# Performance work log

Hardware: AMD Instinct MI355X
Metric: run time of the kernel (lower is better)

The kernel has to match this reference:

```python
import jax, jax.numpy as jnp
import numpy as np

T, L, H, C, D_IN, ED, N, E = 4, 3, 1, 256, 20, 10, 4096, 65536
D = H * C  # 256, pooling width
AH = 4     # pooling attention heads


def setup_inputs() -> dict:
    key = jax.random.key(0)
    ks = jax.random.split(key, 24)
    g = lambda k, s, sc=0.05: jax.random.normal(k, s, jnp.float32) * sc
    return {
        "x": jax.random.normal(ks[0], (N, D_IN), jnp.float32),
        "src": jax.random.randint(ks[1], (E,), 0, N),
        "dst": jax.random.randint(ks[2], (E,), 0, N),
        "edge_attr": jax.random.normal(ks[3], (E, ED), jnp.float32),
        "edge_type": jax.random.randint(ks[4], (E,), 0, T),
        # GATConv params per (edge_type, layer)
        "W0": g(ks[5], (T, D_IN, H * C)),          # layer 0 lin
        "W12": g(ks[6], (T, 2, H * C, H * C)),     # layers 1,2 lin
        "att_src": g(ks[7], (T, L, H, C)),
        "att_dst": g(ks[8], (T, L, H, C)),
        "att_edge": g(ks[9], (T, L, H, C)),
        "lin_edge_w": g(ks[10], (T, L, ED, H * C)),
        "biases": g(ks[11], (T, L, C)),            # H=1 so concat/mean both give C
        "edge_type_weights": jnp.ones((T,), jnp.float32) / T,
        # pooling: MultiheadAttention(D, 4 heads)
        "in_proj_w": g(ks[12], (3 * D, D)),
        "in_proj_b": g(ks[13], (3 * D,)),
        "out_proj_w": g(ks[14], (D, D)),
        "out_proj_b": g(ks[15], (D,)),
        # fusion MLP: 3D -> 2D -> 256
        "fus_w1": g(ks[16], (3 * D, 2 * D)),
        "fus_b1": g(ks[17], (2 * D,)),
        "fus_w2": g(ks[18], (2 * D, 256)),
        "fus_b2": g(ks[19], (256,)),
    }


def _gat(h, src, dst, mask, e_attr, W, a_s, a_d, a_e, We, b, concat):
    # PyG GATConv (edge_dim, add_self_loops=True, fill_value='mean'), eval mode
    Nn = h.shape[0]
    Hh, Cc = a_s.shape
    xl = (h @ W).reshape(Nn, Hh, Cc)
    s_src = jnp.sum(xl * a_s, -1)   # [N,H]
    s_dst = jnp.sum(xl * a_d, -1)   # [N,H]
    s_e = jnp.sum((e_attr @ We).reshape(-1, Hh, Cc) * a_e, -1)  # [E,H]
    # self-loop edge_attr = per-node mean of masked incoming edge_attr
    m = mask.astype(h.dtype)
    cnt = jax.ops.segment_sum(m, dst, Nn)
    loop_attr = jax.ops.segment_sum(e_attr * m[:, None], dst, Nn) / jnp.maximum(cnt, 1.0)[:, None]
    s_loop = jnp.sum((loop_attr @ We).reshape(Nn, Hh, Cc) * a_e, -1)  # [N,H]
    a_real = jax.nn.leaky_relu(s_src[src] + s_dst[dst] + s_e, 0.2)
    a_real = jnp.where(mask[:, None], a_real, -1e30)  # mask edges not of this type
    a_loop = jax.nn.leaky_relu(s_src + s_dst + s_loop, 0.2)
    ar = jnp.arange(Nn)
    idx = jnp.concatenate([dst, ar])    # destination of each (edge + self-loop)
    sidx = jnp.concatenate([src, ar])   # source of each
    scores = jnp.concatenate([a_real, a_loop], 0)  # [E+N, H]
    smax = jax.ops.segment_max(scores, idx, Nn)
    ex = jnp.exp(scores - smax[idx])
    ssum = jax.ops.segment_sum(ex, idx, Nn)
    alpha = ex / (ssum[idx] + 1e-16)
    out = jax.ops.segment_sum(xl[sidx] * alpha[:, :, None], idx, Nn)  # [N,H,C]
    out = out.reshape(Nn, Hh * Cc) if concat else out.mean(1)
    return out + b


def reference(x, src, dst, edge_attr, edge_type, W0, W12, att_src, att_dst,
              att_edge, lin_edge_w, biases, edge_type_weights, in_proj_w,
              in_proj_b, out_proj_w, out_proj_b, fus_w1, fus_b1, fus_w2, fus_b2):
    outs = []
    for t in range(T):
        mask = edge_type == t
        h = x
        for i in range(L):
            W = W0[t] if i == 0 else W12[t, i - 1]
            h = _gat(h, src, dst, mask, edge_attr, W, att_src[t, i],
                     att_dst[t, i], att_edge[t, i], lin_edge_w[t, i],
                     biases[t, i], concat=(i < L - 1))
            h = jax.nn.elu(h)  # dropout off in eval
        outs.append(h)
    w = jax.nn.softmax(edge_type_weights)
    h = sum(w[t] * outs[t] for t in range(T))  # [N, D]
    # HierarchicalGraphPooling
    mean_p = h.mean(0)
    max_p = h.max(0)
    qkv = h @ in_proj_w.T + in_proj_b
    q, k, v = jnp.split(qkv, 3, axis=-1)
    HD = D // AH
    q = q.reshape(-1, AH, HD)
    k = k.reshape(-1, AH, HD)
    v = v.reshape(-1, AH, HD)
    att = jax.nn.softmax(jnp.einsum('nhd,mhd->hnm', q, k) / np.float32(np.sqrt(HD)), axis=-1)
    o = jnp.einsum('hnm,mhd->nhd', att, v).reshape(-1, D) @ out_proj_w.T + out_proj_b
    attn_p = o.mean(0)
    comb = jnp.concatenate([mean_p, max_p, attn_p])  # [3D]
    g = jax.nn.relu(comb @ fus_w1 + fus_b1)
    g = jax.nn.relu(g @ fus_w2 + fus_b2)
    return g[None, :]
```

## Files before the change

### kernel.cpp

```cpp
#include <hip/hip_runtime.h>
#include <math.h>

#define T 4
#define LL 3
#define C 256
#define DIN 20
#define NN 4096
#define EE 65536
#define AHD 4
#define MCH 8
#define QKS 72
#define AST 264
#define SLOTN (16384*64)

#define W_CURSOR 0
#define W_SLSRC  16384
#define F_SLSE   (W_SLSRC + SLOTN)
#define F_XL     (F_SLSE + 3*SLOTN)
#define F_H      (F_XL + T*NN*C)
#define F_OPART  F_XL
#define F_SSRC   (F_H + T*NN*C)
#define F_SDST   (F_SSRC + T*NN)
#define F_WE     (F_SDST + T*NN)
#define F_HACC   (F_WE + 128)
#define F_WT     (F_HACC + NN*C)
#define F_QKV    (F_WT + 768*256)
#define F_DPART  (F_QKV + NN*768)
#define F_MEANP  (F_DPART + MCH*NN*AHD)
#define F_MAXP   (F_MEANP + C)
#define F_OMEAN  (F_MAXP + C)
#define F_ATTNP  (F_OMEAN + C)
#define F_G1     (F_ATTNP + C)
#define U_W12P   (F_G1 + 512)
#define WS_WORDS (U_W12P + 262144)

static __device__ __forceinline__ float lrelu(float x){ return x > 0.f ? x : 0.2f*x; }
static __device__ __forceinline__ float eluf(float x){ return x > 0.f ? x : __expf(x) - 1.f; }

typedef _Float16 half2_t __attribute__((ext_vector_type(2)));
typedef _Float16 v8h __attribute__((ext_vector_type(8)));
typedef float v4f __attribute__((ext_vector_type(4)));

static __device__ __forceinline__ unsigned pk2(float x, float y){
  half2_t h; h.x = (_Float16)x; h.y = (_Float16)y;
  return __builtin_bit_cast(unsigned, h);
}

static __device__ inline void atomicMaxF(float* addr, float val){
  int* ai = (int*)addr;
  int old = __float_as_int(*addr);
  while (__int_as_float(old) < val){
    int assumed = old;
    old = atomicCAS(ai, assumed, __float_as_int(val));
    if (old == assumed) break;
  }
}

__global__ __launch_bounds__(256) void prep_k(
    const float* __restrict__ x, const float* __restrict__ W0,
    const float* __restrict__ attS, const float* __restrict__ attD,
    float* __restrict__ xlo, float* __restrict__ ssrc, float* __restrict__ sdst,
    const float* __restrict__ w12, _Float16* __restrict__ wpT,
    const float* __restrict__ ipw, _Float16* __restrict__ ip16,
    const float* __restrict__ linE, const float* __restrict__ attE,
    float* we, float* fbase, int* cursor){
  __shared__ float smem[64*65];
  __shared__ float red[64];
  int by = blockIdx.y, bx = blockIdx.x, tid = threadIdx.x;
  if (by < 4){
    int t = by;
    const float* W = W0 + (size_t)t*DIN*C;
    int n0 = bx*8;
    for (int j = 0; j < 8; j++)
      for (int k = tid; k < DIN; k += 256)
        smem[j*DIN + k] = x[(n0+j)*DIN + k];
    __syncthreads();
    float acc[8] = {0,0,0,0,0,0,0,0};
    int c = tid;
    for (int k = 0; k < DIN; k += 4){
      float w0 = W[(k+0)*C + c], w1 = W[(k+1)*C + c], w2 = W[(k+2)*C + c], w3 = W[(k+3)*C + c];
      #pragma unroll
      for (int j = 0; j < 8; j++){
        float4 h4 = *(const float4*)&smem[j*DIN + k];
        acc[j] += w0*h4.x + w1*h4.y + w2*h4.z + w3*h4.w;
      }
    }
    #pragma unroll
    for (int j = 0; j < 8; j++) xlo[((size_t)t*NN + n0 + j)*C + c] = acc[j];
    float aS = attS[t*LL*C + c], aD = attD[t*LL*C + c];
    int lane = c & 63, w = c >> 6;
    #pragma unroll
    for (int j = 0; j < 8; j++){
      float v1 = acc[j]*aS, v2 = acc[j]*aD;
      #pragma unroll
      for (int off = 32; off > 0; off >>= 1){ v1 += __shfl_down(v1, off); v2 += __shfl_down(v2, off); }
      if (lane == 0){ red[j*8 + w] = v1; red[j*8 + 4 + w] = v2; }
    }
    __syncthreads();
    if (c < 16){
      int j = c >> 1, which = c & 1;
      const float* r = red + j*8 + which*4;
      float s = r[0] + r[1] + r[2] + r[3];
      (which ? sdst : ssrc)[t*NN + n0 + j] = s;
    }
  } else if (by < 12){
    if (bx < 16){
      int b8 = by - 4;
      int k0 = (bx >> 2)*64, n0 = (bx & 3)*64;
      const float* src = w12 + ((size_t)b8*256 + k0)*256 + n0;
      int row = tid >> 2, l4 = (tid & 3)*4;
      #pragma unroll
      for (int pass = 0; pass < 4; pass++){
        float4 v = *(const float4*)(src + (size_t)row*256 + pass*16 + l4);
        int o = row*65 + pass*16 + l4;
        smem[o+0] = v.x; smem[o+1] = v.y; smem[o+2] = v.z; smem[o+3] = v.w;
      }
      __syncthreads();
      int n = tid >> 2, seg = tid & 3;
      _Float16* dstp = wpT + ((size_t)b8*256 + n0 + n)*256 + k0 + seg*16;
      v8h h0, h1;
      #pragma unroll
      for (int i = 0; i < 8; i++) h0[i] = (_Float16)smem[(seg*16 + i)*65 + n];
      #pragma unroll
      for (int i = 0; i < 8; i++) h1[i] = (_Float16)smem[(seg*16 + 8 + i)*65 + n];
      *(v8h*)(dstp) = h0;
      *(v8h*)(dstp + 8) = h1;
    }
  } else if (by < 15){
    if (bx < 256){
      int j = (by - 12)*256 + bx;
      ip16[(size_t)j*256 + tid] = (_Float16)ipw[(size_t)j*256 + tid];
    }
  } else {
    if (bx < 12){
      int t = bx / 3, l = bx % 3;
      float ae = attE[(t*LL + l)*C + tid];
      const float* lw = linE + (size_t)((t*LL + l)*10)*C;
      for (int k = 0; k < 10; k++) smem[k*C + tid] = lw[k*C + tid]*ae;
      __syncthreads();
      if (tid < 10){
        float s = 0.f;
        for (int i = 0; i < C; i++) s += smem[tid*C + i];
        we[(t*LL + l)*10 + tid] = s;
      }
    } else if (bx == 12){
      fbase[tid] = 0.f;
      fbase[256 + tid] = -1e30f;
      fbase[512 + tid] = 0.f;
    } else if (bx >= 64 && bx < 128){
      cursor[(bx - 64)*256 + tid] = 0;
    }
  }
}

__global__ __launch_bounds__(256) void scat_k(const int* __restrict__ dst, const int* __restrict__ ety,
                                              const int* __restrict__ srcv, const float* __restrict__ eattr,
                                              const float* __restrict__ we,
                                              int* cursor, int* slot_src, float* slot_se){
  int e = blockIdx.x*256 + threadIdx.x;
  if (e < EE){
    int t = ety[e];
    int gid = dst[e]*T + t;
    int p = atomicAdd(&cursor[gid], 1);
    if (p < 64){
      int sl = gid*64 + p;
      slot_src[sl] = srcv[e];
      float ea[10];
      #pragma unroll
      for (int k = 0; k < 10; k++) ea[k] = eattr[(size_t)e*10 + k];
      #pragma unroll
      for (int l = 0; l < 3; l++){
        const float* w = we + (t*LL + l)*10;
        float s = 0.f;
        #pragma unroll
        for (int k = 0; k < 10; k++) s += ea[k]*w[k];
        slot_se[(size_t)l*SLOTN + sl] = s;
      }
    }
  }
}

__global__ __launch_bounds__(256, 2) void gemm16m_k(const float* __restrict__ hin,
                                                    const _Float16* __restrict__ wpT,
                                                    const float* __restrict__ attS, const float* __restrict__ attD,
                                                    int l, float* __restrict__ xlo,
                                                    float* __restrict__ ssrc, float* __restrict__ sdst){
  __shared__ __align__(16) _Float16 As[64*AST];
  __shared__ float redS[4*64], redD[4*64];
  int t = blockIdx.y;
  int mb = blockIdx.x*64;
  int tid = threadIdx.x;
  int w = tid >> 6, lane = tid & 63;
  int r16 = lane & 15, q = lane >> 4;
  const float* h = hin + ((size_t)t*NN + mb)*C;
  {
    int sr = tid >> 2, sc = (tid & 3)*64;
    const float* hr = h + (size_t)sr*C + sc;
    #pragma unroll
    for (int i = 0; i < 8; i++){
      float4 a = *(const float4*)(hr + 8*i);
      float4 b = *(const float4*)(hr + 8*i + 4);
      v8h hv = {(_Float16)a.x,(_Float16)a.y,(_Float16)a.z,(_Float16)a.w,
                (_Float16)b.x,(_Float16)b.y,(_Float16)b.z,(_Float16)b.w};
      *(v8h*)(As + (size_t)sr*AST + sc + 8*i) = hv;
    }
  }
  __syncthreads();
  int cb = w*64;
  const _Float16* WB = wpT + ((size_t)((t*2 + (l-1))*256 + cb))*256;
  v4f o[4][4];
  #pragma unroll
  for (int i = 0; i < 4; i++)
    #pragma unroll
    for (int j = 0; j < 4; j++) o[i][j] = (v4f){0.f,0.f,0.f,0.f};
  #pragma unroll
  for (int kk = 0; kk < 8; kk++){
    v8h a[4], b[4];
    #pragma unroll
    for (int mi = 0; mi < 4; mi++) a[mi] = *(v8h*)(As + (size_t)(mi*16 + r16)*AST + kk*32 + q*8);
    #pragma unroll
    for (int ni = 0; ni < 4; ni++) b[ni] = *(const v8h*)(WB + (size_t)(ni*16 + r16)*256 + kk*32 + q*8);
    #pragma unroll
    for (int mi = 0; mi < 4; mi++)
      #pragma unroll
      for (int ni = 0; ni < 4; ni++)
        o[mi][ni] = __builtin_amdgcn_mfma_f32_16x16x32_f16(a[mi], b[ni], o[mi][ni], 0, 0, 0);
  }
  int tl = t*LL + l;
  float aS[4], aD[4];
  #pragma unroll
  for (int ni = 0; ni < 4; ni++){
    aS[ni] = attS[tl*C + cb + ni*16 + r16];
    aD[ni] = attD[tl*C + cb + ni*16 + r16];
  }
  #pragma unroll
  for (int mi = 0; mi < 4; mi++)
    #pragma unroll
    for (int rr = 0; rr < 4; rr++){
      int row = mb + mi*16 + q*4 + rr;
      float v1 = 0.f, v2 = 0.f;
      #pragma unroll
      for (int ni = 0; ni < 4; ni++){
        float ov = o[mi][ni][rr];
        xlo[((size_t)t*NN + row)*C + cb + ni*16 + r16] = ov;
        v1 += ov*aS[ni]; v2 += ov*aD[ni];
      }
      v1 += __shfl_xor(v1, 1); v2 += __shfl_xor(v2, 1);
      v1 += __shfl_xor(v1, 2); v2 += __shfl_xor(v2, 2);
      v1 += __shfl_xor(v1, 4); v2 += __shfl_xor(v2, 4);
      v1 += __shfl_xor(v1, 8); v2 += __shfl_xor(v2, 8);
      if (r16 == 0){
        redS[w*64 + mi*16 + q*4 + rr] = v1;
        redD[w*64 + mi*16 + q*4 + rr] = v2;
      }
    }
  __syncthreads();
  if (tid < 64)
    ssrc[t*NN + mb + tid] = redS[tid] + redS[64+tid] + redS[128+tid] + redS[192+tid];
  else if (tid < 128){
    int i = tid - 64;
    sdst[t*NN + mb + i] = redD[i] + redD[64+i] + redD[128+i] + redD[192+i];
  }
}

__global__ __launch_bounds__(256, 2) void qkv16m_k(const float* __restrict__ hacc,
                                                   const _Float16* __restrict__ ip16,
                                                   const float* __restrict__ ipb, float* __restrict__ qkv,
                                                   float* meanp, float* maxp){
  __shared__ __align__(16) _Float16 As[64*AST];
  int p = blockIdx.y;
  int mb = blockIdx.x*64;
  int tid = threadIdx.x;
  int w = tid >> 6, lane = tid & 63;
  int r16 = lane & 15, q = lane >> 4;
  {
    int sr = tid >> 2, sc = (tid & 3)*64;
    const float* hr = hacc + ((size_t)(mb + sr))*C + sc;
    #pragma unroll
    for (int i = 0; i < 8; i++){
      float4 a = *(const float4*)(hr + 8*i);
      float4 b = *(const float4*)(hr + 8*i + 4);
      v8h hv = {(_Float16)a.x,(_Float16)a.y,(_Float16)a.z,(_Float16)a.w,
                (_Float16)b.x,(_Float16)b.y,(_Float16)b.z,(_Float16)b.w};
      *(v8h*)(As + (size_t)sr*AST + sc + 8*i) = hv;
    }
  }
  __syncthreads();
  int cb = p*256 + w*64;
  v4f o[4][4];
  #pragma unroll
  for (int i = 0; i < 4; i++)
    #pragma unroll
    for (int j = 0; j < 4; j++) o[i][j] = (v4f){0.f,0.f,0.f,0.f};
  #pragma unroll
  for (int kk = 0; kk < 8; kk++){
    v8h a[4], b[4];
    #pragma unroll
    for (int mi = 0; mi < 4; mi++) a[mi] = *(v8h*)(As + (size_t)(mi*16 + r16)*AST + kk*32 + q*8);
    #pragma unroll
    for (int ni = 0; ni < 4; ni++) b[ni] = *(const v8h*)(ip16 + (size_t)(cb + ni*16 + r16)*256 + kk*32 + q*8);
    #pragma unroll
    for (int mi = 0; mi < 4; mi++)
      #pragma unroll
      for (int ni = 0; ni < 4; ni++)
        o[mi][ni] = __builtin_amdgcn_mfma_f32_16x16x32_f16(a[mi], b[ni], o[mi][ni], 0, 0, 0);
  }
  float bn[4];
  #pragma unroll
  for (int ni = 0; ni < 4; ni++) bn[ni] = ipb[cb + ni*16 + r16];
  #pragma unroll
  for (int mi = 0; mi < 4; mi++)
    #pragma unroll
    for (int rr = 0; rr < 4; rr++){
      int row = mb + mi*16 + q*4 + rr;
      #pragma unroll
      for (int ni = 0; ni < 4; ni++)
        qkv[(size_t)row*768 + cb + ni*16 + r16] = o[mi][ni][rr] + bn[ni];
    }
  if (p == 0){
    float sm = 0.f, mx = -1e30f;
    for (int r = 0; r < 64; r++){
      float v = hacc[(size_t)(mb + r)*C + tid];
      sm += v; mx = fmaxf(mx, v);
    }
    atomicAdd(&meanp[tid], sm*(1.f/4096.f));
    atomicMaxF(&maxp[tid], mx);
  }
}

__global__ __launch_bounds__(256) void agg_k(const float* __restrict__ xl, const float* __restrict__ ssrc,
                                             const float* __restrict__ sdst,
                                             const int* __restrict__ cnt, const int* __restrict__ slot_src,
                                             const float* __restrict__ slot_se,
                                             const float* __restrict__ bias, float* __restrict__ hout,
                                             const float* __restrict__ etw, float* __restrict__ hacc, int l){
  __shared__ float4 sh[4][64];
  int gid = blockIdx.x*4 + (threadIdx.x >> 6);
  int lane = threadIdx.x & 63;
  int n = gid >> 2, t = gid & 3;
  int deg = cnt[gid];
  if (deg > 64) deg = 64;
  float sd = sdst[t*NN + n];
  float se_e = 0.f; int sj = 0;
  if (lane < deg){
    int sl = gid*64 + lane;
    sj = slot_src[sl];
    se_e = slot_se[(size_t)l*SLOTN + sl];
  }
  float ssum_se = se_e;
  #pragma unroll
  for (int o = 32; o > 0; o >>= 1) ssum_se += __shfl_xor(ssum_se, o);
  float sloop = ssum_se / (float)(deg > 0 ? deg : 1);
  float sc = (lane < deg) ? lrelu(ssrc[t*NN + sj] + sd + se_e) : -1e30f;
  float al = lrelu(ssrc[t*NN + n] + sd + sloop);
  float mx = fmaxf(sc, al);
  #pragma unroll
  for (int o = 32; o > 0; o >>= 1) mx = fmaxf(mx, __shfl_xor(mx, o));
  float ex = (lane < deg) ? __expf(sc - mx) : 0.f;
  float ale = __expf(al - mx);
  float ssum = ex;
  #pragma unroll
  for (int o = 32; o > 0; o >>= 1) ssum += __shfl_xor(ssum, o);
  float inv = 1.f/(ssum + ale + 1e-16f);
  const float4* xl4 = (const float4*)xl;
  float4 acc = xl4[((size_t)(t*NN + n))*64 + lane];
  acc.x *= ale; acc.y *= ale; acc.z *= ale; acc.w *= ale;
  int dmax = deg - 1;
  for (int j0 = 0; j0 < deg; j0 += 4){
    float p0 = __shfl(ex, j0);
    float p1 = (j0+1 < deg) ? __shfl(ex, j0+1) : 0.f;
    float p2 = (j0+2 < deg) ? __shfl(ex, j0+2) : 0.f;
    float p3 = (j0+3 < deg) ? __shfl(ex, j0+3) : 0.f;
    int s0 = __shfl(sj, j0);
    int s1 = __shfl(sj, (j0+1 < deg) ? j0+1 : dmax);
    int s2 = __shfl(sj, (j0+2 < deg) ? j0+2 : dmax);
    int s3 = __shfl(sj, (j0+3 < deg) ? j0+3 : dmax);
    float4 v0 = xl4[((size_t)(t*NN + s0))*64 + lane];
    float4 v1 = xl4[((size_t)(t*NN + s1))*64 + lane];
    float4 v2 = xl4[((size_t)(t*NN + s2))*64 + lane];
    float4 v3 = xl4[((size_t)(t*NN + s3))*64 + lane];
    acc.x += p0*v0.x + p1*v1.x + p2*v2.x + p3*v3.x;
    acc.y += p0*v0.y + p1*v1.y + p2*v2.y + p3*v3.y;
    acc.z += p0*v0.z + p1*v1.z + p2*v2.z + p3*v3.z;
    acc.w += p0*v0.w + p1*v1.w + p2*v2.w + p3*v3.w;
  }
  float4 b4 = *(const float4*)&bias[(t*LL + l)*C + lane*4];
  acc.x = eluf(acc.x*inv + b4.x); acc.y = eluf(acc.y*inv + b4.y);
  acc.z = eluf(acc.z*inv + b4.z); acc.w = eluf(acc.w*inv + b4.w);
  if (l < 2){
    ((float4*)hout)[((size_t)(t*NN + n))*64 + lane] = acc;
  } else {
    sh[t][lane] = acc;
    __syncthreads();
    if (t == 0){
      float e0 = etw[0], e1 = etw[1], e2 = etw[2], e3 = etw[3];
      float m = fmaxf(fmaxf(e0,e1), fmaxf(e2,e3));
      float w0 = __expf(e0-m), w1 = __expf(e1-m), w2 = __expf(e2-m), w3 = __expf(e3-m);
      float winv = 1.f/(w0+w1+w2+w3);
      float4 v0 = sh[0][lane], v1 = sh[1][lane], v2 = sh[2][lane], v3 = sh[3][lane];
      float4 s;
      s.x = (w0*v0.x + w1*v1.x + w2*v2.x + w3*v3.x)*winv;
      s.y = (w0*v0.y + w1*v1.y + w2*v2.y + w3*v3.y)*winv;
      s.z = (w0*v0.z + w1*v1.z + w2*v2.z + w3*v3.z)*winv;
      s.w = (w0*v0.w + w1*v1.w + w2*v2.w + w3*v3.w)*winv;
      ((float4*)hacc)[(size_t)n*64 + lane] = s;
    }
  }
}

__global__ __launch_bounds__(256, 2) void attn_k(const float* __restrict__ qkv,
                                                 float* __restrict__ opart,
                                                 float* __restrict__ dpart){
  __shared__ __align__(16) _Float16 Ks[64*QKS];
  __shared__ __align__(16) _Float16 VTs[64*QKS];
  __shared__ __align__(16) _Float16 Ps[4][64*QKS];
  int tid = threadIdx.x;
  int wave = tid >> 6, l = tid & 63;
  int nb = blockIdx.x*256 + wave*64;
  int h = blockIdx.y, mc = blockIdx.z;
  int r16 = l & 15, q = l >> 4;
  _Float16* Pw = Ps[wave];

  v8h qf[4][2];
  #pragma unroll
  for (int ni = 0; ni < 4; ni++){
    const float* qrow = qkv + (size_t)(nb + ni*16 + r16)*768 + h*64;
    #pragma unroll
    for (int kk = 0; kk < 2; kk++){
      float4 a = *(const float4*)(qrow + kk*32 + q*8);
      float4 b = *(const float4*)(qrow + kk*32 + q*8 + 4);
      v8h hv = {(_Float16)(a.x*0.125f), (_Float16)(a.y*0.125f),
                (_Float16)(a.z*0.125f), (_Float16)(a.w*0.125f),
                (_Float16)(b.x*0.125f), (_Float16)(b.y*0.125f),
                (_Float16)(b.z*0.125f), (_Float16)(b.w*0.125f)};
      qf[ni][kk] = hv;
    }
  }

  v4f o[4][4];
  #pragma unroll
  for (int i = 0; i < 4; i++)
    #pragma unroll
    for (int j = 0; j < 4; j++) o[i][j] = (v4f){0.f,0.f,0.f,0.f};
  float dn[4] = {0.f,0.f,0.f,0.f};

  for (int mt = 0; mt < NN/MCH/64; mt++){
    int mb = mc*(NN/MCH) + mt*64;
    __syncthreads();
    {
      int sr = tid >> 2, sc = (tid & 3)*16;
      const float* krow = qkv + (size_t)(mb + sr)*768 + 256 + h*64 + sc;
      float4 a = *(const float4*)(krow + 0);
      float4 b = *(const float4*)(krow + 4);
      float4 cc = *(const float4*)(krow + 8);
      float4 d = *(const float4*)(krow + 12);
      v8h h0 = {(_Float16)a.x, (_Float16)a.y, (_Float16)a.z, (_Float16)a.w,
                (_Float16)b.x, (_Float16)b.y, (_Float16)b.z, (_Float16)b.w};
      v8h h1 = {(_Float16)cc.x, (_Float16)cc.y, (_Float16)cc.z, (_Float16)cc.w,
                (_Float16)d.x, (_Float16)d.y, (_Float16)d.z, (_Float16)d.w};
      *(v8h*)(Ks + (size_t)sr*QKS + sc) = h0;
      *(v8h*)(Ks + (size_t)sr*QKS + sc + 8) = h1;
    }
    {
      int m0 = (tid & 31)*2;
      int db = (tid >> 5)*8;
      const float* v0 = qkv + (size_t)(mb + m0)*768 + 512 + h*64 + db;
      const float* v1 = v0 + 768;
      #pragma unroll
      for (int i = 0; i < 2; i++){
        float4 a = *(const float4*)(v0 + 4*i);
        float4 b = *(const float4*)(v1 + 4*i);
        int d = db + 4*i;
        *(unsigned*)(VTs + (size_t)(d+0)*QKS + m0) = pk2(a.x, b.x);
        *(unsigned*)(VTs + (size_t)(d+1)*QKS + m0) = pk2(a.y, b.y);
        *(unsigned*)(VTs + (size_t)(d+2)*QKS + m0) = pk2(a.z, b.z);
        *(unsigned*)(VTs + (size_t)(d+3)*QKS + m0) = pk2(a.w, b.w);
      }
    }
    __syncthreads();
    v4f c[4][4];
    #pragma unroll
    for (int i = 0; i < 4; i++)
      #pragma unroll
      for (int j = 0; j < 4; j++) c[i][j] = (v4f){0.f,0.f,0.f,0.f};
    #pragma unroll
    for (int kk = 0; kk < 2; kk++){
      v8h a[4];
      #pragma unroll
      for (int mi = 0; mi < 4; mi++) a[mi] = *(v8h*)(Ks + (size_t)(mi*16 + r16)*QKS + kk*32 + q*8);
      #pragma unroll
      for (int mi = 0; mi < 4; mi++)
        #pragma unroll
        for (int ni = 0; ni < 4; ni++)
          c[mi][ni] = __builtin_amdgcn_mfma_f32_16x16x32_f16(a[mi], qf[ni][kk], c[mi][ni], 0, 0, 0);
    }
    #pragma unroll
    for (int mi = 0; mi < 4; mi++)
      #pragma unroll
      for (int ni = 0; ni < 4; ni++){
        float e0 = __expf(c[mi][ni][0]), e1 = __expf(c[mi][ni][1]),
              e2 = __expf(c[mi][ni][2]), e3 = __expf(c[mi][ni][3]);
        dn[ni] += e0 + e1 + e2 + e3;
        *(uint2*)(Pw + (size_t)(ni*16 + r16)*QKS + mi*16 + q*4) = make_uint2(pk2(e0,e1), pk2(e2,e3));
      }
    #pragma unroll
    for (int km = 0; km < 2; km++){
      v8h pa[4], vb[4];
      #pragma unroll
      for (int ni = 0; ni < 4; ni++) pa[ni] = *(v8h*)(Pw + (size_t)(ni*16 + r16)*QKS + km*32 + q*8);
      #pragma unroll
      for (int di = 0; di < 4; di++) vb[di] = *(v8h*)(VTs + (size_t)(di*16 + r16)*QKS + km*32 + q*8);
      #pragma unroll
      for (int ni = 0; ni < 4; ni++)
        #pragma unroll
        for (int di = 0; di < 4; di++)
          o[ni][di] = __builtin_amdgcn_mfma_f32_16x16x32_f16(pa[ni], vb[di], o[ni][di], 0, 0, 0);
    }
  }

  float* ob = opart + ((size_t)mc*NN + nb)*C + h*64;
  #pragma unroll
  for (int ni = 0; ni < 4; ni++)
    #pragma unroll
    for (int di = 0; di < 4; di++)
      #pragma unroll
      for (int r = 0; r < 4; r++)
        ob[(size_t)(ni*16 + q*4 + r)*C + di*16 + r16] = o[ni][di][r];
  #pragma unroll
  for (int ni = 0; ni < 4; ni++){
    dn[ni] += __shfl_xor(dn[ni], 16);
    dn[ni] += __shfl_xor(dn[ni], 32);
  }
  if (q == 0){
    #pragma unroll
    for (int ni = 0; ni < 4; ni++)
      dpart[((size_t)mc*NN + nb + ni*16 + r16)*AHD + h] = dn[ni];
  }
}

__global__ __launch_bounds__(256) void attnred_k(const float* __restrict__ opart, const float* __restrict__ dpart,
                                                 float* omean){
  int r0 = blockIdx.x*(NN/256), c = threadIdx.x;
  int head = c >> 6;
  float s = 0.f;
  for (int r = 0; r < NN/256; r++){
    int n = r0 + r;
    float dsum = 0.f, osum = 0.f;
    #pragma unroll
    for (int mc = 0; mc < MCH; mc++){
      dsum += dpart[((size_t)mc*NN + n)*AHD + head];
      osum += opart[((size_t)mc*NN + n)*C + c];
    }
    s += osum / (dsum + 1e-16f);
  }
  atomicAdd(&omean[c], s*(1.f/4096.f));
}

__global__ __launch_bounds__(256) void taila_k(const float* __restrict__ omean, const float* __restrict__ opw,
                                               const float* __restrict__ opb, const float* __restrict__ fb1,
                                               float* attnp, float* g1){
  __shared__ float sh[256];
  int tid = threadIdx.x;
  sh[tid] = omean[tid];
  __syncthreads();
  int jj = tid >> 4, kk = tid & 15;
  int j = blockIdx.x*16 + jj;
  float acc = 0.f;
  #pragma unroll
  for (int i = 0; i < 16; i++){
    int k = kk*16 + i;
    acc += sh[k]*opw[(size_t)j*256 + k];
  }
  acc += __shfl_xor(acc, 1); acc += __shfl_xor(acc, 2);
  acc += __shfl_xor(acc, 4); acc += __shfl_xor(acc, 8);
  if (kk == 0) attnp[j] = acc + opb[j];
  if (blockIdx.x < 2) g1[blockIdx.x*256 + tid] = fb1[blockIdx.x*256 + tid];
}

__global__ __launch_bounds__(512) void tailb_k(const float* __restrict__ meanp, const float* __restrict__ maxp,
                                               const float* __restrict__ attnp, const float* __restrict__ fw1,
                                               float* g1){
  __shared__ float comb[48];
  int b = blockIdx.x, tid = threadIdx.x;
  if (tid < 48){
    int k = b*48 + tid;
    comb[tid] = (k < 256) ? meanp[k] : (k < 512 ? maxp[k-256] : attnp[k-512]);
  }
  __syncthreads();
  float acc = 0.f;
  #pragma unroll 4
  for (int i = 0; i < 48; i++)
    acc += comb[i]*fw1[((size_t)(b*48 + i))*512 + tid];
  atomicAdd(&g1[tid], acc);
}

__global__ __launch_bounds__(256) void tailc_k(const float* __restrict__ g1, const float* __restrict__ fw2,
                                               const float* __restrict__ fb2, float* __restrict__ out){
  __shared__ float g[512];
  __shared__ float red[256];
  int tid = threadIdx.x;
  g[tid] = fmaxf(g1[tid], 0.f);
  g[tid + 256] = fmaxf(g1[tid + 256], 0.f);
  __syncthreads();
  int j = blockIdx.x*32 + (tid & 31);
  int kp = tid >> 5;
  float acc = 0.f;
  #pragma unroll 4
  for (int i = 0; i < 64; i++){
    int k = kp*64 + i;
    acc += g[k]*fw2[(size_t)k*256 + j];
  }
  red[tid] = acc;
  __syncthreads();
  if (tid < 32){
    float s = 0.f;
    #pragma unroll
    for (int p = 0; p < 8; p++) s += red[p*32 + tid];
    out[j] = fmaxf(s + fb2[j], 0.f);
  }
}

extern "C" void kernel_launch(void* const* d_in, const int* in_sizes, int n_in,
                              void* d_out, int out_size, void* d_ws, size_t ws_size,
                              hipStream_t stream){
  const float* x     = (const float*)d_in[0];
  const int*   srcv  = (const int*)d_in[1];
  const int*   dstv  = (const int*)d_in[2];
  const float* eattr = (const float*)d_in[3];
  const int*   etyp  = (const int*)d_in[4];
  const float* W0    = (const float*)d_in[5];
  const float* W12   = (const float*)d_in[6];
  const float* attS  = (const float*)d_in[7];
  const float* attD  = (const float*)d_in[8];
  const float* attE  = (const float*)d_in[9];
  const float* linE  = (const float*)d_in[10];
  const float* bias  = (const float*)d_in[11];
  const float* etw   = (const float*)d_in[12];
  const float* ipw   = (const float*)d_in[13];
  const float* ipb   = (const float*)d_in[14];
  const float* opw   = (const float*)d_in[15];
  const float* opb   = (const float*)d_in[16];
  const float* fw1   = (const float*)d_in[17];
  const float* fb1   = (const float*)d_in[18];
  const float* fw2   = (const float*)d_in[19];
  const float* fb2   = (const float*)d_in[20];
  float* out = (float*)d_out;

  if (ws_size < (size_t)WS_WORDS*4) return;

  int*       ip   = (int*)d_ws;
  float*     fp   = (float*)d_ws;
  _Float16*  ip16 = (_Float16*)(fp + F_WT);
  _Float16*  wpT  = (_Float16*)(fp + U_W12P);

  prep_k<<<dim3(512, 16), 256, 0, stream>>>(x, W0, attS, attD,
                                            fp + F_XL, fp + F_SSRC, fp + F_SDST,
                                            W12, wpT, ipw, ip16, linE, attE,
                                            fp + F_WE, fp + F_MEANP, ip + W_CURSOR);

  scat_k<<<EE/256, 256, 0, stream>>>(dstv, etyp, srcv, eattr, fp + F_WE,
                                     ip + W_CURSOR, ip + W_SLSRC, fp + F_SLSE);

  agg_k<<<(NN*T)/4, 256, 0, stream>>>(fp + F_XL, fp + F_SSRC, fp + F_SDST,
                                      ip + W_CURSOR, ip + W_SLSRC, fp + F_SLSE,
                                      bias, fp + F_H, etw, fp + F_HACC, 0);
  for (int l = 1; l < 3; l++){
    gemm16m_k<<<dim3(NN/64, T), 256, 0, stream>>>(fp + F_H, wpT, attS, attD, l,
                                                  fp + F_XL, fp + F_SSRC, fp + F_SDST);
    agg_k<<<(NN*T)/4, 256, 0, stream>>>(fp + F_XL, fp + F_SSRC, fp + F_SDST,
                                        ip + W_CURSOR, ip + W_SLSRC, fp + F_SLSE,
                                        bias, fp + F_H, etw, fp + F_HACC, l);
  }

  qkv16m_k<<<dim3(NN/64, 3), 256, 0, stream>>>(fp + F_HACC, ip16, ipb, fp + F_QKV,
                                               fp + F_MEANP, fp + F_MAXP);
  attn_k<<<dim3(NN/256, AHD, MCH), 256, 0, stream>>>(fp + F_QKV, fp + F_OPART, fp + F_DPART);

  attnred_k<<<256, 256, 0, stream>>>(fp + F_OPART, fp + F_DPART, fp + F_OMEAN);
  taila_k<<<16, 256, 0, stream>>>(fp + F_OMEAN, opw, opb, fb1, fp + F_ATTNP, fp + F_G1);
  tailb_k<<<16, 512, 0, stream>>>(fp + F_MEANP, fp + F_MAXP, fp + F_ATTNP, fw1, fp + F_G1);
  tailc_k<<<8, 256, 0, stream>>>(fp + F_G1, fw2, fb2, out);
}
```

Measured before the change: 289.4 us.

## Store intermediate activations in fp16 across GAT, QKV and attention kernels

Measured after the change: 268.3 us. -7.3%, faster.

```diff
diff --git a/kernel.cpp b/kernel.cpp
--- a/kernel.cpp
+++ b/kernel.cpp
@@ -17,15 +17,15 @@
 #define W_SLSRC  16384
 #define F_SLSE   (W_SLSRC + SLOTN)
 #define F_XL     (F_SLSE + 3*SLOTN)
-#define F_H      (F_XL + T*NN*C)
+#define F_H      (F_XL + T*NN*C/2)
 #define F_OPART  F_XL
-#define F_SSRC   (F_H + T*NN*C)
+#define F_SSRC   (F_H + T*NN*C/2)
 #define F_SDST   (F_SSRC + T*NN)
 #define F_WE     (F_SDST + T*NN)
 #define F_HACC   (F_WE + 128)
-#define F_WT     (F_HACC + NN*C)
-#define F_QKV    (F_WT + 768*256)
-#define F_DPART  (F_QKV + NN*768)
+#define F_WT     (F_HACC + NN*C/2)
+#define F_QKV    (F_WT + 768*256/2)
+#define F_DPART  (F_QKV + NN*768/2)
 #define F_MEANP  (F_DPART + MCH*NN*AHD)
 #define F_MAXP   (F_MEANP + C)
 #define F_OMEAN  (F_MAXP + C)
@@ -45,6 +45,18 @@
   half2_t h; h.x = (_Float16)x; h.y = (_Float16)y;
   return __builtin_bit_cast(unsigned, h);
 }
+static __device__ __forceinline__ unsigned pk2h(_Float16 x, _Float16 y){
+  half2_t h; h.x = x; h.y = y;
+  return __builtin_bit_cast(unsigned, h);
+}
+static __device__ __forceinline__ float4 up4(uint2 u){
+  half2_t a = __builtin_bit_cast(half2_t, u.x);
+  half2_t b = __builtin_bit_cast(half2_t, u.y);
+  return make_float4((float)a.x, (float)a.y, (float)b.x, (float)b.y);
+}
+static __device__ __forceinline__ uint2 dn4(float4 v){
+  return make_uint2(pk2(v.x, v.y), pk2(v.z, v.w));
+}
 
 static __device__ inline void atomicMaxF(float* addr, float val){
   int* ai = (int*)addr;
@@ -59,7 +71,7 @@
 __global__ __launch_bounds__(256) void prep_k(
     const float* __restrict__ x, const float* __restrict__ W0,
     const float* __restrict__ attS, const float* __restrict__ attD,
-    float* __restrict__ xlo, float* __restrict__ ssrc, float* __restrict__ sdst,
+    _Float16* __restrict__ xlo, float* __restrict__ ssrc, float* __restrict__ sdst,
     const float* __restrict__ w12, _Float16* __restrict__ wpT,
     const float* __restrict__ ipw, _Float16* __restrict__ ip16,
     const float* __restrict__ linE, const float* __restrict__ attE,
@@ -86,7 +98,7 @@
       }
     }
     #pragma unroll
-    for (int j = 0; j < 8; j++) xlo[((size_t)t*NN + n0 + j)*C + c] = acc[j];
+    for (int j = 0; j < 8; j++) xlo[((size_t)t*NN + n0 + j)*C + c] = (_Float16)acc[j];
     float aS = attS[t*LL*C + c], aD = attD[t*LL*C + c];
     int lane = c & 63, w = c >> 6;
     #pragma unroll
@@ -180,10 +192,10 @@
   }
 }
 
-__global__ __launch_bounds__(256, 2) void gemm16m_k(const float* __restrict__ hin,
+__global__ __launch_bounds__(256, 2) void gemm16m_k(const _Float16* __restrict__ hin,
                                                     const _Float16* __restrict__ wpT,
                                                     const float* __restrict__ attS, const float* __restrict__ attD,
-                                                    int l, float* __restrict__ xlo,
+                                                    int l, _Float16* __restrict__ xlo,
                                                     float* __restrict__ ssrc, float* __restrict__ sdst){
   __shared__ __align__(16) _Float16 As[64*AST];
   __shared__ float redS[4*64], redD[4*64];
@@ -192,18 +204,12 @@
   int tid = threadIdx.x;
   int w = tid >> 6, lane = tid & 63;
   int r16 = lane & 15, q = lane >> 4;
-  const float* h = hin + ((size_t)t*NN + mb)*C;
   {
     int sr = tid >> 2, sc = (tid & 3)*64;
-    const float* hr = h + (size_t)sr*C + sc;
-    #pragma unroll
-    for (int i = 0; i < 8; i++){
-      float4 a = *(const float4*)(hr + 8*i);
-      float4 b = *(const float4*)(hr + 8*i + 4);
-      v8h hv = {(_Float16)a.x,(_Float16)a.y,(_Float16)a.z,(_Float16)a.w,
-                (_Float16)b.x,(_Float16)b.y,(_Float16)b.z,(_Float16)b.w};
-      *(v8h*)(As + (size_t)sr*AST + sc + 8*i) = hv;
-    }
+    const _Float16* hr = hin + ((size_t)(t*NN + mb + sr))*C + sc;
+    #pragma unroll
+    for (int i = 0; i < 8; i++)
+      *(v8h*)(As + (size_t)sr*AST + sc + 8*i) = *(const v8h*)(hr + 8*i);
   }
   __syncthreads();
   int cb = w*64;
@@ -242,7 +248,7 @@
       #pragma unroll
       for (int ni = 0; ni < 4; ni++){
         float ov = o[mi][ni][rr];
-        xlo[((size_t)t*NN + row)*C + cb + ni*16 + r16] = ov;
+        xlo[((size_t)t*NN + row)*C + cb + ni*16 + r16] = (_Float16)ov;
         v1 += ov*aS[ni]; v2 += ov*aD[ni];
       }
       v1 += __shfl_xor(v1, 1); v2 += __shfl_xor(v2, 1);
@@ -263,9 +269,9 @@
   }
 }
 
-__global__ __launch_bounds__(256, 2) void qkv16m_k(const float* __restrict__ hacc,
+__global__ __launch_bounds__(256, 2) void qkv16m_k(const _Float16* __restrict__ hacc,
                                                    const _Float16* __restrict__ ip16,
-                                                   const float* __restrict__ ipb, float* __restrict__ qkv,
+                                                   const float* __restrict__ ipb, _Float16* __restrict__ qkv,
                                                    float* meanp, float* maxp){
   __shared__ __align__(16) _Float16 As[64*AST];
   int p = blockIdx.y;
@@ -275,15 +281,10 @@
   int r16 = lane & 15, q = lane >> 4;
   {
     int sr = tid >> 2, sc = (tid & 3)*64;
-    const float* hr = hacc + ((size_t)(mb + sr))*C + sc;
-    #pragma unroll
-    for (int i = 0; i < 8; i++){
-      float4 a = *(const float4*)(hr + 8*i);
-      float4 b = *(const float4*)(hr + 8*i + 4);
-      v8h hv = {(_Float16)a.x,(_Float16)a.y,(_Float16)a.z,(_Float16)a.w,
-                (_Float16)b.x,(_Float16)b.y,(_Float16)b.z,(_Float16)b.w};
-      *(v8h*)(As + (size_t)sr*AST + sc + 8*i) = hv;
-    }
+    const _Float16* hr = hacc + ((size_t)(mb + sr))*C + sc;
+    #pragma unroll
+    for (int i = 0; i < 8; i++)
+      *(v8h*)(As + (size_t)sr*AST + sc + 8*i) = *(const v8h*)(hr + 8*i);
   }
   __syncthreads();
   int cb = p*256 + w*64;
@@ -315,12 +316,12 @@
       int row = mb + mi*16 + q*4 + rr;
       #pragma unroll
       for (int ni = 0; ni < 4; ni++)
-        qkv[(size_t)row*768 + cb + ni*16 + r16] = o[mi][ni][rr] + bn[ni];
+        qkv[(size_t)row*768 + cb + ni*16 + r16] = (_Float16)(o[mi][ni][rr] + bn[ni]);
     }
   if (p == 0){
     float sm = 0.f, mx = -1e30f;
     for (int r = 0; r < 64; r++){
-      float v = hacc[(size_t)(mb + r)*C + tid];
+      float v = (float)hacc[(size_t)(mb + r)*C + tid];
       sm += v; mx = fmaxf(mx, v);
     }
     atomicAdd(&meanp[tid], sm*(1.f/4096.f));
@@ -328,12 +329,12 @@
   }
 }
 
-__global__ __launch_bounds__(256) void agg_k(const float* __restrict__ xl, const float* __restrict__ ssrc,
+__global__ __launch_bounds__(256) void agg_k(const _Float16* __restrict__ xl, const float* __restrict__ ssrc,
                                              const float* __restrict__ sdst,
                                              const int* __restrict__ cnt, const int* __restrict__ slot_src,
                                              const float* __restrict__ slot_se,
-                                             const float* __restrict__ bias, float* __restrict__ hout,
-                                             const float* __restrict__ etw, float* __restrict__ hacc, int l){
+                                             const float* __restrict__ bias, _Float16* __restrict__ hout,
+                                             const float* __restrict__ etw, _Float16* __restrict__ hacc, int l){
   __shared__ float4 sh[4][64];
   int gid = blockIdx.x*4 + (threadIdx.x >> 6);
   int lane = threadIdx.x & 63;
@@ -362,8 +363,8 @@
   #pragma unroll
   for (int o = 32; o > 0; o >>= 1) ssum += __shfl_xor(ssum, o);
   float inv = 1.f/(ssum + ale + 1e-16f);
-  const float4* xl4 = (const float4*)xl;
-  float4 acc = xl4[((size_t)(t*NN + n))*64 + lane];
+  const uint2* xl2 = (const uint2*)xl;
+  float4 acc = up4(xl2[((size_t)(t*NN + n))*64 + lane]);
   acc.x *= ale; acc.y *= ale; acc.z *= ale; acc.w *= ale;
   int dmax = deg - 1;
   for (int j0 = 0; j0 < deg; j0 += 4){
@@ -375,10 +376,10 @@
     int s1 = __shfl(sj, (j0+1 < deg) ? j0+1 : dmax);
     int s2 = __shfl(sj, (j0+2 < deg) ? j0+2 : dmax);
     int s3 = __shfl(sj, (j0+3 < deg) ? j0+3 : dmax);
-    float4 v0 = xl4[((size_t)(t*NN + s0))*64 + lane];
-    float4 v1 = xl4[((size_t)(t*NN + s1))*64 + lane];
-    float4 v2 = xl4[((size_t)(t*NN + s2))*64 + lane];
-    float4 v3 = xl4[((size_t)(t*NN + s3))*64 + lane];
+    float4 v0 = up4(xl2[((size_t)(t*NN + s0))*64 + lane]);
+    float4 v1 = up4(xl2[((size_t)(t*NN + s1))*64 + lane]);
+    float4 v2 = up4(xl2[((size_t)(t*NN + s2))*64 + lane]);
+    float4 v3 = up4(xl2[((size_t)(t*NN + s3))*64 + lane]);
     acc.x += p0*v0.x + p1*v1.x + p2*v2.x + p3*v3.x;
     acc.y += p0*v0.y + p1*v1.y + p2*v2.y + p3*v3.y;
     acc.z += p0*v0.z + p1*v1.z + p2*v2.z + p3*v3.z;
@@ -388,7 +389,7 @@
   acc.x = eluf(acc.x*inv + b4.x); acc.y = eluf(acc.y*inv + b4.y);
   acc.z = eluf(acc.z*inv + b4.z); acc.w = eluf(acc.w*inv + b4.w);
   if (l < 2){
-    ((float4*)hout)[((size_t)(t*NN + n))*64 + lane] = acc;
+    ((uint2*)hout)[((size_t)(t*NN + n))*64 + lane] = dn4(acc);
   } else {
     sh[t][lane] = acc;
     __syncthreads();
@@ -403,13 +404,13 @@
       s.y = (w0*v0.y + w1*v1.y + w2*v2.y + w3*v3.y)*winv;
       s.z = (w0*v0.z + w1*v1.z + w2*v2.z + w3*v3.z)*winv;
       s.w = (w0*v0.w + w1*v1.w + w2*v2.w + w3*v3.w)*winv;
-      ((float4*)hacc)[(size_t)n*64 + lane] = s;
-    }
-  }
-}
-
-__global__ __launch_bounds__(256, 2) void attn_k(const float* __restrict__ qkv,
-                                                 float* __restrict__ opart,
+      ((uint2*)hacc)[(size_t)n*64 + lane] = dn4(s);
+    }
+  }
+}
+
+__global__ __launch_bounds__(256, 2) void attn_k(const _Float16* __restrict__ qkv,
+                                                 _Float16* __restrict__ opart,
                                                  float* __restrict__ dpart){
   __shared__ __align__(16) _Float16 Ks[64*QKS];
   __shared__ __align__(16) _Float16 VTs[64*QKS];
@@ -424,15 +425,12 @@
   v8h qf[4][2];
   #pragma unroll
   for (int ni = 0; ni < 4; ni++){
-    const float* qrow = qkv + (size_t)(nb + ni*16 + r16)*768 + h*64;
+    const _Float16* qrow = qkv + (size_t)(nb + ni*16 + r16)*768 + h*64;
     #pragma unroll
     for (int kk = 0; kk < 2; kk++){
-      float4 a = *(const float4*)(qrow + kk*32 + q*8);
-      float4 b = *(const float4*)(qrow + kk*32 + q*8 + 4);
-      v8h hv = {(_Float16)(a.x*0.125f), (_Float16)(a.y*0.125f),
-                (_Float16)(a.z*0.125f), (_Float16)(a.w*0.125f),
-                (_Float16)(b.x*0.125f), (_Float16)(b.y*0.125f),
-                (_Float16)(b.z*0.125f), (_Float16)(b.w*0.125f)};
+      v8h hv = *(const v8h*)(qrow + kk*32 + q*8);
+      #pragma unroll
+      for (int i = 0; i < 8; i++) hv[i] = hv[i] * (_Float16)0.125f;
       qf[ni][kk] = hv;
     }
   }
@@ -449,33 +447,20 @@
     __syncthreads();
     {
       int sr = tid >> 2, sc = (tid & 3)*16;
-      const float* krow = qkv + (size_t)(mb + sr)*768 + 256 + h*64 + sc;
-      float4 a = *(const float4*)(krow + 0);
-      float4 b = *(const float4*)(krow + 4);
-      float4 cc = *(const float4*)(krow + 8);
-      float4 d = *(const float4*)(krow + 12);
-      v8h h0 = {(_Float16)a.x, (_Float16)a.y, (_Float16)a.z, (_Float16)a.w,
-                (_Float16)b.x, (_Float16)b.y, (_Float16)b.z, (_Float16)b.w};
-      v8h h1 = {(_Float16)cc.x, (_Float16)cc.y, (_Float16)cc.z, (_Float16)cc.w,
-                (_Float16)d.x, (_Float16)d.y, (_Float16)d.z, (_Float16)d.w};
-      *(v8h*)(Ks + (size_t)sr*QKS + sc) = h0;
-      *(v8h*)(Ks + (size_t)sr*QKS + sc + 8) = h1;
+      const _Float16* krow = qkv + (size_t)(mb + sr)*768 + 256 + h*64 + sc;
+      *(v8h*)(Ks + (size_t)sr*QKS + sc) = *(const v8h*)(krow);
+      *(v8h*)(Ks + (size_t)sr*QKS + sc + 8) = *(const v8h*)(krow + 8);
     }
     {
       int m0 = (tid & 31)*2;
       int db = (tid >> 5)*8;
-      const float* v0 = qkv + (size_t)(mb + m0)*768 + 512 + h*64 + db;
-      const float* v1 = v0 + 768;
-      #pragma unroll
-      for (int i = 0; i < 2; i++){
-        float4 a = *(const float4*)(v0 + 4*i);
-        float4 b = *(const float4*)(v1 + 4*i);
-        int d = db + 4*i;
-        *(unsigned*)(VTs + (size_t)(d+0)*QKS + m0) = pk2(a.x, b.x);
-        *(unsigned*)(VTs + (size_t)(d+1)*QKS + m0) = pk2(a.y, b.y);
-        *(unsigned*)(VTs + (size_t)(d+2)*QKS + m0) = pk2(a.z, b.z);
-        *(unsigned*)(VTs + (size_t)(d+3)*QKS + m0) = pk2(a.w, b.w);
-      }
+      const _Float16* v0 = qkv + (size_t)(mb + m0)*768 + 512 + h*64 + db;
+      const _Float16* v1 = v0 + 768;
+      v8h a = *(const v8h*)v0;
+      v8h b = *(const v8h*)v1;
+      #pragma unroll
+      for (int d = 0; d < 8; d++)
+        *(unsigned*)(VTs + (size_t)(db+d)*QKS + m0) = pk2h(a[d], b[d]);
     }
     __syncthreads();
     v4f c[4][4];
@@ -518,14 +503,14 @@
     }
   }
 
-  float* ob = opart + ((size_t)mc*NN + nb)*C + h*64;
+  _Float16* ob = opart + ((size_t)mc*NN + nb)*C + h*64;
   #pragma unroll
   for (int ni = 0; ni < 4; ni++)
     #pragma unroll
     for (int di = 0; di < 4; di++)
       #pragma unroll
       for (int r = 0; r < 4; r++)
-        ob[(size_t)(ni*16 + q*4 + r)*C + di*16 + r16] = o[ni][di][r];
+        ob[(size_t)(ni*16 + q*4 + r)*C + di*16 + r16] = (_Float16)o[ni][di][r];
   #pragma unroll
   for (int ni = 0; ni < 4; ni++){
     dn[ni] += __shfl_xor(dn[ni], 16);
@@ -538,7 +523,7 @@
   }
 }
 
-__global__ __launch_bounds__(256) void attnred_k(const float* __restrict__ opart, const float* __restrict__ dpart,
+__global__ __launch_bounds__(256) void attnred_k(const _Float16* __restrict__ opart, const float* __restrict__ dpart,
                                                  float* omean){
   int r0 = blockIdx.x*(NN/256), c = threadIdx.x;
   int head = c >> 6;
@@ -549,7 +534,7 @@
     #pragma unroll
     for (int mc = 0; mc < MCH; mc++){
       dsum += dpart[((size_t)mc*NN + n)*AHD + head];
-      osum += opart[((size_t)mc*NN + n)*C + c];
+      osum += (float)opart[((size_t)mc*NN + n)*C + c];
     }
     s += osum / (dsum + 1e-16f);
   }
@@ -648,35 +633,40 @@
 
   if (ws_size < (size_t)WS_WORDS*4) return;
 
-  int*       ip   = (int*)d_ws;
-  float*     fp   = (float*)d_ws;
-  _Float16*  ip16 = (_Float16*)(fp + F_WT);
-  _Float16*  wpT  = (_Float16*)(fp + U_W12P);
+  int*       ip    = (int*)d_ws;
+  float*     fp    = (float*)d_ws;
+  _Float16*  xl16  = (_Float16*)(fp + F_XL);
+  _Float16*  h16   = (_Float16*)(fp + F_H);
+  _Float16*  op16  = (_Float16*)(fp + F_OPART);
+  _Float16*  hacc16= (_Float16*)(fp + F_HACC);
+  _Float16*  ip16  = (_Float16*)(fp + F_WT);
+  _Float16*  qkv16 = (_Float16*)(fp + F_QKV);
+  _Float16*  wpT   = (_Float16*)(fp + U_W12P);
 
   prep_k<<<dim3(512, 16), 256, 0, stream>>>(x, W0, attS, attD,
-                                            fp + F_XL, fp + F_SSRC, fp + F_SDST,
+                                            xl16, fp + F_SSRC, fp + F_SDST,
                                             W12, wpT, ipw, ip16, linE, attE,
                                             fp + F_WE, fp + F_MEANP, ip + W_CURSOR);
 
   scat_k<<<EE/256, 256, 0, stream>>>(dstv, etyp, srcv, eattr, fp + F_WE,
                                      ip + W_CURSOR, ip + W_SLSRC, fp + F_SLSE);
 
-  agg_k<<<(NN*T)/4, 256, 0, stream>>>(fp + F_XL, fp + F_SSRC, fp + F_SDST,
+  agg_k<<<(NN*T)/4, 256, 0, stream>>>(xl16, fp + F_SSRC, fp + F_SDST,
                                       ip + W_CURSOR, ip + W_SLSRC, fp + F_SLSE,
-                                      bias, fp + F_H, etw, fp + F_HACC, 0);
+                                      bias, h16, etw, hacc16, 0);
   for (int l = 1; l < 3; l++){
-    gemm16m_k<<<dim3(NN/64, T), 256, 0, stream>>>(fp + F_H, wpT, attS, attD, l,
-                                                  fp + F_XL, fp + F_SSRC, fp + F_SDST);
-    agg_k<<<(NN*T)/4, 256, 0, stream>>>(fp + F_XL, fp + F_SSRC, fp + F_SDST,
+    gemm16m_k<<<dim3(NN/64, T), 256, 0, stream>>>(h16, wpT, attS, attD, l,
+                                                  xl16, fp + F_SSRC, fp + F_SDST);
+    agg_k<<<(NN*T)/4, 256, 0, stream>>>(xl16, fp + F_SSRC, fp + F_SDST,
                                         ip + W_CURSOR, ip + W_SLSRC, fp + F_SLSE,
-                                        bias, fp + F_H, etw, fp + F_HACC, l);
-  }
-
-  qkv16m_k<<<dim3(NN/64, 3), 256, 0, stream>>>(fp + F_HACC, ip16, ipb, fp + F_QKV,
+                                        bias, h16, etw, hacc16, l);
+  }
+
+  qkv16m_k<<<dim3(NN/64, 3), 256, 0, stream>>>(hacc16, ip16, ipb, qkv16,
                                                fp + F_MEANP, fp + F_MAXP);
-  attn_k<<<dim3(NN/256, AHD, MCH), 256, 0, stream>>>(fp + F_QKV, fp + F_OPART, fp + F_DPART);
-
-  attnred_k<<<256, 256, 0, stream>>>(fp + F_OPART, fp + F_DPART, fp + F_OMEAN);
+  attn_k<<<dim3(NN/256, AHD, MCH), 256, 0, stream>>>(qkv16, op16, fp + F_DPART);
+
+  attnred_k<<<256, 256, 0, stream>>>(op16, fp + F_DPART, fp + F_OMEAN);
   taila_k<<<16, 256, 0, stream>>>(fp + F_OMEAN, opw, opb, fb1, fp + F_ATTNP, fp + F_G1);
   tailb_k<<<16, 512, 0, stream>>>(fp + F_MEANP, fp + F_MAXP, fp + F_ATTNP, fw1, fp + F_G1);
   tailc_k<<<8, 256, 0, stream>>>(fp + F_G1, fw2, fb2, out);
```
